# Performance work log

Hardware: AMD Instinct MI355X
Metric: run time of the kernel (lower is better)

The kernel has to match this reference:

```python
import jax, jax.numpy as jnp
import numpy as np

N, E, G, F, H, L, NH, HD = 40000, 640000, 256, 9, 128, 3, 4, 32
EPS = 1e-5

def _ln(x, g, b):
    m = jnp.mean(x, axis=-1, keepdims=True)
    v = jnp.mean((x - m) ** 2, axis=-1, keepdims=True)
    return (x - m) * jax.lax.rsqrt(v + EPS) * g + b

def _forward(floats, edge_index, batch):
    (x, pos, emb_w, emb_b, edge_w1, edge_b1, edge_w2, edge_b2,
     node_w1, node_b1, node_w2, node_b2, qkv_w, qkv_b, out_w, out_b,
     ln1_g, ln1_b, ln2_g, ln2_b, ff_w1, ff_b1, ff_w2, ff_b2,
     cls_w1, cls_b1, cls_w2, cls_b2) = floats
    src, dst = edge_index[0], edge_index[1]  # PyG: x_j = x[src], x_i = x[dst], aggregate at dst
    dist = jnp.linalg.norm(pos[dst] - pos[src], axis=-1, keepdims=True)  # [E,1]
    h = x @ emb_w + emb_b  # [N,H]
    for l in range(L):
        # message: edge_mlp(cat[x_i, x_j, dist])
        ef = jnp.concatenate([h[dst], h[src], dist], axis=-1)  # [E,2H+1]
        m = jax.nn.silu(ef @ edge_w1[l] + edge_b1[l])
        m = jax.nn.silu(m @ edge_w2[l] + edge_b2[l])  # [E,H]
        aggr = jax.ops.segment_sum(m, dst, num_segments=N)  # [N,H]
        u = jax.nn.silu(jnp.concatenate([h, aggr], axis=-1) @ node_w1[l] + node_b1[l])
        u = u @ node_w2[l] + node_b2[l]
        h = h + u  # residual in GAHT.forward
    # per-graph mean pooling (faithful to masked-mean loop)
    sums = jax.ops.segment_sum(h, batch, num_segments=G)  # [G,H]
    cnts = jax.ops.segment_sum(jnp.ones((N,), h.dtype), batch, num_segments=G)
    g = sums / jnp.maximum(cnts, 1.0)[:, None]  # [G,H]
    # 2-layer post-norm transformer encoder (batch=1, seq=G), relu FFN, eval mode (no dropout)
    scale = 1.0 / jnp.sqrt(jnp.asarray(HD, g.dtype))
    for t in range(2):
        qkv = g @ qkv_w[t] + qkv_b[t]  # [G,3H]
        q, k, v = jnp.split(qkv, 3, axis=-1)
        q = q.reshape(G, NH, HD); k = k.reshape(G, NH, HD); v = v.reshape(G, NH, HD)
        att = jax.nn.softmax(jnp.einsum('qhd,khd->hqk', q, k) * scale, axis=-1)
        o = jnp.einsum('hqk,khd->qhd', att, v).reshape(G, H)
        o = o @ out_w[t] + out_b[t]
        g = _ln(g + o, ln1_g[t], ln1_b[t])
        ff = jax.nn.relu(g @ ff_w1[t] + ff_b1[t]) @ ff_w2[t] + ff_b2[t]
        g = _ln(g + ff, ln2_g[t], ln2_b[t])
    out = jax.nn.relu(g @ cls_w1 + cls_b1) @ cls_w2 + cls_b2  # [G,1]
    return out.squeeze(-1)  # [G]


def setup_inputs() -> dict:
    key = jax.random.key(0)
    ks = jax.random.split(key, 16)
    def p(k, shape, scale=0.08):
        return jax.random.normal(k, shape, dtype=jnp.float32) * scale
    return {
        'x': jax.random.normal(ks[0], (N, F), dtype=jnp.float32),
        'pos': jax.random.normal(ks[1], (N, 3), dtype=jnp.float32),
        'emb_w': p(ks[2], (F, H)), 'emb_b': jnp.zeros((H,), jnp.float32),
        'edge_w1': p(ks[3], (L, 2 * H + 1, H)), 'edge_b1': jnp.zeros((L, H), jnp.float32),
        'edge_w2': p(ks[4], (L, H, H)), 'edge_b2': jnp.zeros((L, H), jnp.float32),
        'node_w1': p(ks[5], (L, 2 * H, H)), 'node_b1': jnp.zeros((L, H), jnp.float32),
        'node_w2': p(ks[6], (L, H, H)), 'node_b2': jnp.zeros((L, H), jnp.float32),
        'qkv_w': p(ks[7], (2, H, 3 * H)), 'qkv_b': jnp.zeros((2, 3 * H), jnp.float32),
        'out_w': p(ks[8], (2, H, H)), 'out_b': jnp.zeros((2, H), jnp.float32),
        'ln1_g': jnp.ones((2, H), jnp.float32), 'ln1_b': jnp.zeros((2, H), jnp.float32),
        'ln2_g': jnp.ones((2, H), jnp.float32), 'ln2_b': jnp.zeros((2, H), jnp.float32),
        'ff_w1': p(ks[9], (2, H, 2 * H)), 'ff_b1': jnp.zeros((2, 2 * H), jnp.float32),
        'ff_w2': p(ks[10], (2, 2 * H, H)), 'ff_b2': jnp.zeros((2, H), jnp.float32),
        'cls_w1': p(ks[11], (H, H // 2)), 'cls_b1': jnp.zeros((H // 2,), jnp.float32),
        'cls_w2': p(ks[12], (H // 2, 1)), 'cls_b2': jnp.zeros((1,), jnp.float32),
        'edge_index': jax.random.randint(ks[13], (2, E), 0, N),
        'batch': jnp.sort(jax.random.randint(ks[14], (N,), 0, G)),
    }


def reference(x, pos, emb_w, emb_b, edge_w1, edge_b1, edge_w2, edge_b2,
              node_w1, node_b1, node_w2, node_b2, qkv_w, qkv_b, out_w, out_b,
              ln1_g, ln1_b, ln2_g, ln2_b, ff_w1, ff_b1, ff_w2, ff_b2,
              cls_w1, cls_b1, cls_w2, cls_b2, edge_index, batch):
    floats = (x, pos, emb_w, emb_b, edge_w1, edge_b1, edge_w2, edge_b2,
              node_w1, node_b1, node_w2, node_b2, qkv_w, qkv_b, out_w, out_b,
              ln1_g, ln1_b, ln2_g, ln2_b, ff_w1, ff_b1, ff_w2, ff_b2,
              cls_w1, cls_b1, cls_w2, cls_b2)
    return _forward(floats, edge_index, batch)
```

## Files before the change

### kernel.cpp

```cpp
#include <hip/hip_runtime.h>
#include <hip/hip_bf16.h>
#include <stdint.h>

#define NN 40000
#define EE 640000
#define GG 256
#define FFE 9
#define HH 128

typedef __bf16 bf16;
typedef __bf16 bf16x8 __attribute__((ext_vector_type(8)));
typedef float f32x4 __attribute__((ext_vector_type(4)));

__device__ __forceinline__ f32x4 mfma16(bf16x8 a, bf16x8 b, f32x4 c){
  return __builtin_amdgcn_mfma_f32_16x16x32_bf16(a, b, c, 0, 0, 0);
}
__device__ __forceinline__ float silu_f(float x){
  return x * __builtin_amdgcn_rcpf(1.0f + __expf(-x));
}
__device__ __forceinline__ uint16_t bfb(float x){ bf16 h=(bf16)x; return *(uint16_t*)&h; }
__device__ __forceinline__ int swz(int row, int cb){
  return row*256 + (cb ^ ((row & 7) << 4));
}

__global__ __launch_bounds__(256) void k_prep(
    const float* __restrict__ edge_w1, const float* __restrict__ edge_w2,
    const float* __restrict__ node_w1, const float* __restrict__ node_w2,
    const float* __restrict__ edge_b1,
    const float* __restrict__ x, const float* __restrict__ emb_w,
    const float* __restrict__ emb_b,
    bf16* __restrict__ wcatT, bf16* __restrict__ w2T,
    bf16* __restrict__ nw1T, bf16* __restrict__ nw2T,
    float* __restrict__ bcat, float* __restrict__ h,
    int* __restrict__ cnt)
{
  int b = blockIdx.x, tid = threadIdx.x;
  if (b < 192){
    int l = b/64; int t2 = (b%64)*256 + tid;
    int n = t2 >> 7, k = t2 & 127;
    wcatT[(size_t)l*32768 + n*128 + k] = (bf16)edge_w1[(size_t)l*32896 + k*128 + n];
  } else if (b < 384){
    int lb = b - 192; int l = lb/64; int t2 = (lb%64)*256 + tid;
    int n = t2 >> 7, k = t2 & 127;
    wcatT[(size_t)l*32768 + 16384 + n*128 + k] = (bf16)edge_w1[(size_t)l*32896 + (128+k)*128 + n];
  } else if (b < 576){
    int lb = b - 384; int l = lb/64; int t2 = (lb%64)*256 + tid;
    int n = t2 >> 7, k = t2 & 127;
    w2T[(size_t)l*16384 + n*128 + k] = (bf16)edge_w2[(size_t)l*16384 + k*128 + n];
  } else if (b < 960){
    int lb = b - 576; int l = lb/128; int t2 = (lb%128)*256 + tid;
    int n = t2 >> 8, k = t2 & 255;
    nw1T[(size_t)l*32768 + n*256 + k] = (bf16)node_w1[(size_t)l*32768 + k*128 + n];
  } else if (b < 1152){
    int lb = b - 960; int l = lb/64; int t2 = (lb%64)*256 + tid;
    int n = t2 >> 7, k = t2 & 127;
    nw2T[(size_t)l*16384 + n*128 + k] = (bf16)node_w2[(size_t)l*16384 + k*128 + n];
  } else if (b < 1155){
    int l = b - 1152;
    bcat[l*256 + tid] = (tid < 128) ? edge_b1[l*128 + tid] : 0.0f;
  } else if (b < 1312){
    int i = (b - 1155)*256 + tid;
    if (i < NN) cnt[i] = 0;
  } else {
    int idx = (b - 1312)*256 + tid;
    int n = idx >> 7, f = idx & 127;
    float s = emb_b[f];
    const float* xr = x + n*FFE;
    #pragma unroll
    for (int k=0;k<FFE;++k) s += xr[k]*emb_w[k*HH + f];
    h[idx] = s;
  }
}

__global__ __launch_bounds__(256) void k_hist(const int* __restrict__ dst, int* __restrict__ cnt){
  int e = blockIdx.x*256 + threadIdx.x;
  if (e < EE) atomicAdd(&cnt[dst[e]], 1);
}

__global__ __launch_bounds__(1024) void k_scan(const int* __restrict__ cnt, int* __restrict__ cursor, int n){
  __shared__ int s_wsum[16];
  __shared__ int s_run;
  int tid = threadIdx.x, lane = tid & 63, wv = tid >> 6;
  if (tid == 0) s_run = 0;
  __syncthreads();
  for (int base=0; base<n; base+=4096){
    int i = base + tid*4;
    int c0 = (i  <n)? cnt[i  ] : 0;
    int c1 = (i+1<n)? cnt[i+1] : 0;
    int c2 = (i+2<n)? cnt[i+2] : 0;
    int c3 = (i+3<n)? cnt[i+3] : 0;
    int t0 = c0, t1 = t0+c1, t2 = t1+c2, t3 = t2+c3;
    int xx = t3;
    #pragma unroll
    for (int off=1; off<64; off<<=1){ int t = __shfl_up(xx, off); if (lane>=off) xx += t; }
    if (lane==63) s_wsum[wv] = xx;
    __syncthreads();
    if (wv==0 && lane<16){
      int y = s_wsum[lane];
      #pragma unroll
      for (int off=1; off<16; off<<=1){ int t = __shfl_up(y, off, 16); if (lane>=off) y += t; }
      s_wsum[lane] = y;
    }
    __syncthreads();
    int woff = wv ? s_wsum[wv-1] : 0;
    int run = s_run;
    int eb = run + woff + xx - t3;
    if (i  <n) cursor[i  ] = eb;
    if (i+1<n) cursor[i+1] = eb + t0;
    if (i+2<n) cursor[i+2] = eb + t1;
    if (i+3<n) cursor[i+3] = eb + t2;
    __syncthreads();
    if (tid==0) s_run = run + s_wsum[15];
    __syncthreads();
  }
}

__global__ __launch_bounds__(256) void k_scatter(
    const int* __restrict__ ei, const float* __restrict__ pos,
    int* __restrict__ cursor, int4* __restrict__ rec)
{
  int e = blockIdx.x*256 + threadIdx.x;
  if (e >= EE) return;
  int s = ei[e], d = ei[EE + e];
  int p = atomicAdd(&cursor[d], 1);
  float dx = pos[d*3+0]-pos[s*3+0];
  float dy = pos[d*3+1]-pos[s*3+1];
  float dz = pos[d*3+2]-pos[s*3+2];
  int4 rc; rc.x = s; rc.y = d; rc.z = __float_as_int(sqrtf(dx*dx+dy*dy+dz*dz)); rc.w = 0;
  rec[p] = rc;
}

template<int KTOT, int K1, int ACT, bool A1BF, bool BIAS, bool RESID, bool OBF, bool OF, bool ZAGGR>
__global__ __launch_bounds__(256) void k_gemm(
    const void* __restrict__ a1v, const float* __restrict__ a2,
    const bf16* __restrict__ wt, const float* __restrict__ bias,
    const float* __restrict__ resid, bf16* __restrict__ outb,
    float* __restrict__ outf, int Nw, float* __restrict__ aggr)
{
  constexpr int LDK = 136;
  __shared__ bf16 s_a[128*LDK];
  __shared__ bf16 s_w[64*LDK];
  int tid = threadIdx.x, lane = tid & 63, w = tid >> 6;
  int m0 = blockIdx.x*128, n0 = blockIdx.y*64;
  if (ZAGGR && blockIdx.y == 0){
    int nrows = NN - m0; if (nrows > 128) nrows = 128;
    f32x4 z = {0.f,0.f,0.f,0.f};
    for (int i = tid; i < nrows*32; i += 256)
      *(f32x4*)(aggr + (size_t)m0*128 + (size_t)i*4) = z;
  }
  f32x4 acc[2][4];
  #pragma unroll
  for (int i=0;i<2;++i)
    #pragma unroll
    for (int j=0;j<4;++j)
      #pragma unroll
      for (int r=0;r<4;++r) acc[i][j][r]=0.f;
  int rsel = lane & 15, ksel = (lane>>4)*8;
  int wm = w*32;

  for (int kh=0; kh<KTOT; kh+=128){
    #pragma unroll
    for (int it=0; it<8; ++it){
      int idx = tid + it*256;
      int row = idx >> 4, col = (idx & 15)*8;
      int gc = kh + col;
      int grow = m0 + row; if (grow > NN-1) grow = NN-1;
      bf16x8 vv;
      if (gc < K1){
        if (A1BF){
          vv = *(const bf16x8*)((const bf16*)a1v + (size_t)grow*K1 + gc);
        } else {
          const float* srcp = (const float*)a1v + (size_t)grow*K1 + gc;
          f32x4 u0 = *(const f32x4*)srcp;
          f32x4 u1 = *(const f32x4*)(srcp+4);
          vv[0]=(bf16)u0[0]; vv[1]=(bf16)u0[1]; vv[2]=(bf16)u0[2]; vv[3]=(bf16)u0[3];
          vv[4]=(bf16)u1[0]; vv[5]=(bf16)u1[1]; vv[6]=(bf16)u1[2]; vv[7]=(bf16)u1[3];
        }
      } else {
        const float* srcp = a2 + (size_t)grow*(KTOT-K1) + (gc-K1);
        f32x4 u0 = *(const f32x4*)srcp;
        f32x4 u1 = *(const f32x4*)(srcp+4);
        vv[0]=(bf16)u0[0]; vv[1]=(bf16)u0[1]; vv[2]=(bf16)u0[2]; vv[3]=(bf16)u0[3];
        vv[4]=(bf16)u1[0]; vv[5]=(bf16)u1[1]; vv[6]=(bf16)u1[2]; vv[7]=(bf16)u1[3];
      }
      *(bf16x8*)&s_a[row*LDK + col] = vv;
    }
    #pragma unroll
    for (int it=0; it<4; ++it){
      int idx = tid + it*256;
      int row = idx >> 4, col = (idx & 15)*8;
      *(bf16x8*)&s_w[row*LDK + col] = *(const bf16x8*)(wt + (size_t)(n0+row)*KTOT + kh + col);
    }
    __syncthreads();
    #pragma unroll
    for (int ks=0; ks<4; ++ks){
      int kb = ks*32 + ksel;
      bf16x8 fa0 = *(const bf16x8*)&s_a[(wm+rsel)*LDK + kb];
      bf16x8 fa1 = *(const bf16x8*)&s_a[(wm+16+rsel)*LDK + kb];
      #pragma unroll
      for (int j=0;j<4;++j){
        bf16x8 fb = *(const bf16x8*)&s_w[(j*16+rsel)*LDK + kb];
        acc[0][j]=mfma16(fa0,fb,acc[0][j]);
        acc[1][j]=mfma16(fa1,fb,acc[1][j]);
      }
    }
    __syncthreads();
  }

  #pragma unroll
  for (int i=0;i<2;++i){
    #pragma unroll
    for (int j=0;j<4;++j){
      int col = n0 + j*16 + rsel;
      float bv = BIAS ? bias[col] : 0.0f;
      #pragma unroll
      for (int r=0;r<4;++r){
        int row = m0 + wm + i*16 + 4*(lane>>4) + r;
        if (row < NN){
          float v = acc[i][j][r] + bv;
          if (ACT==1) v = silu_f(v);
          if (RESID) v += resid[(size_t)row*Nw + col];
          if (OBF) outb[(size_t)row*Nw + col] = (bf16)v;
          if (OF)  outf[(size_t)row*Nw + col] = v;
        }
      }
    }
  }
}

template<bool DOP>
__global__ __launch_bounds__(256) void k_node(
    float* h, float* aggr,
    const bf16* __restrict__ nw1t,
    const bf16* __restrict__ nw2t,
    const bf16* __restrict__ wct,
    const float* __restrict__ nb1, const float* __restrict__ nb2,
    const float* __restrict__ bcv,
    bf16* __restrict__ P)
{
  __shared__ bf16 SA[64][132];
  __shared__ bf16 SW[128][72];
  __shared__ bf16 SU[64][132];
  int tid = threadIdx.x, lane = tid & 63, w = tid >> 6;
  int rsel = lane & 15, hi = lane >> 4;
  int m0 = blockIdx.x * 64;
  int urow = w*16 + rsel;
  int grow = m0 + urow;

  f32x4 acc[8];
  #pragma unroll
  for (int nt=0;nt<8;++nt)
    #pragma unroll
    for (int r=0;r<4;++r) acc[nt][r]=0.f;

  for (int kq=0; kq<4; ++kq){
    const float* src = (kq < 2) ? (h + (size_t)m0*128 + kq*64)
                                : (aggr + (size_t)m0*128 + (kq-2)*64);
    #pragma unroll
    for (int it=0; it<2; ++it){
      int g = tid + it*256;
      int row = g >> 3, cg = (g & 7)*8;
      const float* sp = src + (size_t)row*128 + cg;
      f32x4 u0 = *(const f32x4*)sp, u1v = *(const f32x4*)(sp+4);
      bf16x8 vv;
      vv[0]=(bf16)u0[0]; vv[1]=(bf16)u0[1]; vv[2]=(bf16)u0[2]; vv[3]=(bf16)u0[3];
      vv[4]=(bf16)u1v[0]; vv[5]=(bf16)u1v[1]; vv[6]=(bf16)u1v[2]; vv[7]=(bf16)u1v[3];
      *(bf16x8*)&SA[row][cg] = vv;
    }
    #pragma unroll
    for (int it=0; it<4; ++it){
      int g = tid + it*256;
      int row = g >> 3, cg = (g & 7)*8;
      *(bf16x8*)&SW[row][cg] = *(const bf16x8*)(nw1t + (size_t)row*256 + kq*64 + cg);
    }
    __syncthreads();
    #pragma unroll
    for (int ks=0; ks<2; ++ks){
      int kb = ks*32 + hi*8;
      bf16x8 fa = *(const bf16x8*)&SA[w*16 + rsel][kb];
      #pragma unroll
      for (int nt=0;nt<8;++nt){
        bf16x8 fw = *(const bf16x8*)&SW[nt*16 + rsel][kb];
        acc[nt] = mfma16(fw, fa, acc[nt]);
      }
    }
    __syncthreads();
  }

  #pragma unroll
  for (int nt=0;nt<8;++nt){
    int nb = nt*16 + 4*hi;
    f32x4 b4 = *(const f32x4*)(nb1 + nb);
    uint16_t q0 = bfb(silu_f(acc[nt][0] + b4[0]));
    uint16_t q1 = bfb(silu_f(acc[nt][1] + b4[1]));
    uint16_t q2 = bfb(silu_f(acc[nt][2] + b4[2]));
    uint16_t q3 = bfb(silu_f(acc[nt][3] + b4[3]));
    uint2 pk; pk.x = (unsigned)q0 | ((unsigned)q1 << 16); pk.y = (unsigned)q2 | ((unsigned)q3 << 16);
    *(uint2*)&SU[urow][nb] = pk;
  }
  __syncthreads();

  #pragma unroll
  for (int nt=0;nt<8;++nt)
    #pragma unroll
    for (int r=0;r<4;++r) acc[nt][r]=0.f;
  for (int kq=0; kq<2; ++kq){
    #pragma unroll
    for (int it=0; it<4; ++it){
      int g = tid + it*256;
      int row = g >> 3, cg = (g & 7)*8;
      *(bf16x8*)&SW[row][cg] = *(const bf16x8*)(nw2t + (size_t)row*128 + kq*64 + cg);
    }
    __syncthreads();
    #pragma unroll
    for (int ks=0; ks<2; ++ks){
      int kb = ks*32 + hi*8;
      bf16x8 fa = *(const bf16x8*)&SU[w*16 + rsel][kq*64 + kb];
      #pragma unroll
      for (int nt=0;nt<8;++nt){
        bf16x8 fw = *(const bf16x8*)&SW[nt*16 + rsel][kb];
        acc[nt] = mfma16(fw, fa, acc[nt]);
      }
    }
    __syncthreads();
  }

  #pragma unroll
  for (int nt=0;nt<8;++nt){
    int nb = nt*16 + 4*hi;
    f32x4 b4 = *(const f32x4*)(nb2 + nb);
    f32x4 h4 = *(const f32x4*)(h + (size_t)grow*128 + nb);
    f32x4 v;
    #pragma unroll
    for (int r=0;r<4;++r) v[r] = h4[r] + acc[nt][r] + b4[r];
    *(f32x4*)(h + (size_t)grow*128 + nb) = v;
    uint2 pk;
    pk.x = (unsigned)bfb(v[0]) | ((unsigned)bfb(v[1]) << 16);
    pk.y = (unsigned)bfb(v[2]) | ((unsigned)bfb(v[3]) << 16);
    *(uint2*)&SA[urow][nb] = pk;
  }
  __syncthreads();

  if (DOP){
    for (int nh=0; nh<2; ++nh){
      #pragma unroll
      for (int nt=0;nt<8;++nt)
        #pragma unroll
        for (int r=0;r<4;++r) acc[nt][r]=0.f;
      for (int kq=0; kq<2; ++kq){
        #pragma unroll
        for (int it=0; it<4; ++it){
          int g = tid + it*256;
          int row = g >> 3, cg = (g & 7)*8;
          *(bf16x8*)&SW[row][cg] = *(const bf16x8*)(wct + (size_t)(nh*128+row)*128 + kq*64 + cg);
        }
        __syncthreads();
        #pragma unroll
        for (int ks=0; ks<2; ++ks){
          int kb = ks*32 + hi*8;
          bf16x8 fa = *(const bf16x8*)&SA[w*16 + rsel][kq*64 + kb];
          #pragma unroll
          for (int nt=0;nt<8;++nt){
            bf16x8 fw = *(const bf16x8*)&SW[nt*16 + rsel][kb];
            acc[nt] = mfma16(fw, fa, acc[nt]);
          }
        }
        __syncthreads();
      }
      #pragma unroll
      for (int nt=0;nt<8;++nt){
        int nb = nh*128 + nt*16 + 4*hi;
        f32x4 b4 = *(const f32x4*)(bcv + nb);
        uint2 pk;
        pk.x = (unsigned)bfb(acc[nt][0] + b4[0]) | ((unsigned)bfb(acc[nt][1] + b4[1]) << 16);
        pk.y = (unsigned)bfb(acc[nt][2] + b4[2]) | ((unsigned)bfb(acc[nt][3] + b4[3]) << 16);
        *(uint2*)(P + (size_t)grow*256 + nb) = pk;
      }
    }
    f32x4 z = {0.f,0.f,0.f,0.f};
    #pragma unroll
    for (int it=0; it<8; ++it){
      int idx = tid + it*256;
      *(f32x4*)(aggr + (size_t)m0*128 + (size_t)idx*4) = z;
    }
  }
}

__global__ __launch_bounds__(512, 6) void k_edge(
    const bf16* __restrict__ P, const bf16* __restrict__ w2t,
    const float* __restrict__ w1r, const float* __restrict__ b2,
    const int4* __restrict__ rec, float* __restrict__ aggr)
{
  __shared__ char smem[32768];
  __shared__ int s_dst[128];
  __shared__ unsigned s_segidw[32];
  __shared__ int s_segdst[128];
  __shared__ int s_misc[4];
  int tid = threadIdx.x, lane = tid & 63, w = tid >> 6;
  int rsel = lane & 15, hi = lane >> 4;
  int bid = blockIdx.x;
  int swb = (bid & 7) * (EE/128/8) + (bid >> 3);
  int e0 = swb * 128;
  int col = w*16 + rsel;

  bf16x8 fb[4];
  #pragma unroll
  for (int ks=0;ks<4;++ks)
    fb[ks] = *(const bf16x8*)(w2t + (size_t)col*128 + ks*32 + hi*8);

  if (tid == 0){
    s_misc[0] = (e0 == 0) ? -2147483647 : rec[e0-1].y;
    s_misc[1] = (e0 + 128 >= EE) ? -2147483647 : rec[e0+128].y;
  }

  int cq = (tid & 15)*8;
  int er = tid >> 4;
  int4 rc[4];
  #pragma unroll
  for (int it=0; it<4; ++it) rc[it] = rec[e0 + er + it*32];
  uint4 pau[4], pbu[4];
  #pragma unroll
  for (int it=0; it<4; ++it){
    pau[it] = *(const uint4*)(P + ((size_t)rc[it].y << 8) + cq);
    pbu[it] = *(const uint4*)(P + ((size_t)rc[it].x << 8) + 128 + cq);
  }
  if (cq == 0){
    #pragma unroll
    for (int it=0; it<4; ++it) s_dst[er + it*32] = rc[it].y;
  }
  f32x4 wr0 = *(const f32x4*)(w1r + cq);
  f32x4 wr1 = *(const f32x4*)(w1r + cq + 4);
  #pragma unroll
  for (int it=0; it<4; ++it){
    float dist = __int_as_float(rc[it].z);
    bf16x8 mm;
    #pragma unroll
    for (int j=0;j<4;++j){
      unsigned ua = ((const unsigned*)&pau[it])[j];
      unsigned ub = ((const unsigned*)&pbu[it])[j];
      float al = __uint_as_float(ua << 16);
      float ah = __uint_as_float(ua & 0xFFFF0000u);
      float bl = __uint_as_float(ub << 16);
      float bh = __uint_as_float(ub & 0xFFFF0000u);
      float wlo = (j<2) ? wr0[2*j]   : wr1[2*(j-2)];
      float whi = (j<2) ? wr0[2*j+1] : wr1[2*(j-2)+1];
      mm[2*j]   = (bf16)silu_f(al + bl + dist*wlo);
      mm[2*j+1] = (bf16)silu_f(ah + bh + dist*whi);
    }
    *(bf16x8*)(smem + swz(er + it*32, cq*2)) = mm;
  }
  __syncthreads();

  if (w == 0){
    int d0 = s_dst[2*lane], d1 = s_dst[2*lane+1];
    int dm1 = (lane == 0) ? 0 : s_dst[2*lane-1];
    int h0 = (lane == 0) ? 1 : (d0 != dm1);
    int h1 = (d1 != d0);
    int p = h0 + h1, x = p;
    #pragma unroll
    for (int off=1; off<64; off<<=1){ int t = __shfl_up(x, off); if (lane>=off) x += t; }
    int excl = x - p;
    int id0 = excl + h0 - 1;
    int id1 = excl + p - 1;
    uint8_t* sb = (uint8_t*)s_segidw;
    sb[2*lane]   = (uint8_t)id0;
    sb[2*lane+1] = (uint8_t)id1;
    if (h0) s_segdst[id0] = d0;
    if (h1) s_segdst[id1] = d1;
    if (lane == 63) s_misc[2] = id1 + 1;
  }

  f32x4 acc[8];
  #pragma unroll
  for (int mt=0;mt<8;++mt)
    #pragma unroll
    for (int r=0;r<4;++r) acc[mt][r]=0.f;
  #pragma unroll
  for (int mt=0;mt<8;++mt){
    #pragma unroll
    for (int ks=0;ks<4;++ks){
      bf16x8 fa = *(const bf16x8*)(smem + swz(mt*16 + rsel, ks*64 + hi*16));
      acc[mt] = mfma16(fa, fb[ks], acc[mt]);
    }
  }
  __syncthreads();

  float bb = b2[col];
  #pragma unroll
  for (int mt=0;mt<8;++mt){
    uint2 pk;
    pk.x = (unsigned)bfb(silu_f(acc[mt][0] + bb)) | ((unsigned)bfb(silu_f(acc[mt][1] + bb)) << 16);
    pk.y = (unsigned)bfb(silu_f(acc[mt][2] + bb)) | ((unsigned)bfb(silu_f(acc[mt][3] + bb)) << 16);
    *(uint2*)(smem + col*256 + ((mt*32 + hi*8) ^ ((col & 7) << 4))) = pk;
  }
  __syncthreads();

  bf16x8 gb[4];
  #pragma unroll
  for (int ks=0;ks<4;++ks)
    gb[ks] = *(const bf16x8*)(smem + col*256 + ((ks*64 + hi*16) ^ ((col & 7) << 4)));
  int nseg = s_misc[2];
  bool openL = (s_dst[0]   == s_misc[0]);
  bool openR = (s_dst[127] == s_misc[1]);
  for (int st = 0; st < nseg; st += 16){
    unsigned tgt = (unsigned)(st + rsel);
    f32x4 racc = {0.f,0.f,0.f,0.f};
    #pragma unroll
    for (int ks=0;ks<4;++ks){
      unsigned w0 = s_segidw[ks*8 + hi*2];
      unsigned w1 = s_segidw[ks*8 + hi*2 + 1];
      union { uint16_t u[8]; bf16x8 v; } sa;
      #pragma unroll
      for (int j=0;j<4;++j){
        sa.u[j]   = (((w0 >> (8*j)) & 255u) == tgt) ? (uint16_t)0x3F80 : (uint16_t)0;
        sa.u[4+j] = (((w1 >> (8*j)) & 255u) == tgt) ? (uint16_t)0x3F80 : (uint16_t)0;
      }
      racc = mfma16(sa.v, gb[ks], racc);
    }
    #pragma unroll
    for (int r=0;r<4;++r){
      int s = st + 4*hi + r;
      if (s < nseg){
        float v = racc[r];
        size_t off = (size_t)s_segdst[s]*128 + col;
        bool atom = (s == 0 && openL) || (s == nseg-1 && openR);
        if (atom) atomicAdd(&aggr[off], v);
        else      aggr[off] = v;
      }
    }
  }
}

__device__ __forceinline__ int lbound(const int* a, int n, int key){
  int lo=0, hi=n;
  while (lo<hi){ int mid=(lo+hi)>>1; if (a[mid]<key) lo=mid+1; else hi=mid; }
  return lo;
}

__global__ __launch_bounds__(384) void k_pool_qkv(
    const float* __restrict__ h, const int* __restrict__ batch,
    const float* __restrict__ wq, const float* __restrict__ bq,
    float* __restrict__ gbuf, float* __restrict__ qkvb)
{
  __shared__ float sg[128];
  int gr = blockIdx.x, tid = threadIdx.x;
  if (tid < 128){
    int lo = lbound(batch, NN, gr), hi2 = lbound(batch, NN, gr+1);
    float s = 0.f;
    for (int n=lo;n<hi2;++n) s += h[(size_t)n*HH + tid];
    int c = hi2 - lo; if (c < 1) c = 1;
    s /= (float)c;
    sg[tid] = s; gbuf[gr*128 + tid] = s;
  }
  __syncthreads();
  float a = bq[tid];
  for (int k=0;k<128;++k) a += sg[k]*wq[k*384 + tid];
  qkvb[gr*384 + tid] = a;
}

template<int MODE>
__global__ __launch_bounds__(128) void k_tail(
    const float* __restrict__ qkv, const float* __restrict__ wo,
    const float* __restrict__ bo, const float* __restrict__ l1g,
    const float* __restrict__ l1b, const float* __restrict__ w1,
    const float* __restrict__ b1f, const float* __restrict__ w2,
    const float* __restrict__ b2f, const float* __restrict__ l2g,
    const float* __restrict__ l2b, float* __restrict__ gbuf,
    const float* __restrict__ wq2, const float* __restrict__ bq2,
    float* __restrict__ qkvb2,
    const float* __restrict__ cw1, const float* __restrict__ cb1,
    const float* __restrict__ cw2, const float* __restrict__ cb2,
    float* __restrict__ out)
{
  __shared__ float sq[128];
  __shared__ float ss[4][256];
  __shared__ float so[128];
  __shared__ float st[256];
  __shared__ float red[4];
  int r = blockIdx.x, tid = threadIdx.x;
  sq[tid] = qkv[r*384 + tid];
  __syncthreads();
  const float scale = 0.17677669529663687f;
  for (int i=tid; i<1024; i+=128){
    int hh = i >> 8, j = i & 255;
    const float* kr = qkv + j*384 + 128 + hh*32;
    const float* qr = sq + hh*32;
    float s=0;
    #pragma unroll
    for (int d=0;d<32;++d) s += qr[d]*kr[d];
    ss[hh][j] = s*scale;
  }
  __syncthreads();
  int hh = tid >> 5, sl = tid & 31;
  float m = -1e30f;
  #pragma unroll
  for (int q8=0;q8<8;++q8) m = fmaxf(m, ss[hh][sl + q8*32]);
  #pragma unroll
  for (int off=16; off; off>>=1) m = fmaxf(m, __shfl_xor(m, off, 32));
  float sum = 0.f;
  #pragma unroll
  for (int q8=0;q8<8;++q8){
    float e = __expf(ss[hh][sl+q8*32] - m);
    ss[hh][sl+q8*32] = e;
    sum += e;
  }
  #pragma unroll
  for (int off=16; off; off>>=1) sum += __shfl_xor(sum, off, 32);
  float inv = __builtin_amdgcn_rcpf(sum);
  __syncthreads();
  float accv = 0.f;
  for (int j=0;j<256;++j) accv += ss[hh][j]*qkv[j*384 + 256 + hh*32 + sl];
  so[tid] = accv*inv;
  __syncthreads();
  float a = bo[tid];
  for (int k=0;k<128;++k) a += so[k]*wo[k*128 + tid];
  float val = gbuf[r*128 + tid] + a;
  {
    float s = val, q = val*val;
    #pragma unroll
    for (int off=32; off; off>>=1){ s += __shfl_xor(s, off); q += __shfl_xor(q, off); }
    int lane = tid & 63, wv = tid >> 6;
    if (lane==0){ red[wv*2]=s; red[wv*2+1]=q; }
    __syncthreads();
    float S = red[0]+red[2], Q = red[1]+red[3];
    float mean = S*(1.0f/128.0f);
    float var = Q*(1.0f/128.0f) - mean*mean;
    float ninv = rsqrtf(var + 1e-5f);
    val = (val-mean)*ninv*l1g[tid] + l1b[tid];
  }
  sq[tid] = val;
  __syncthreads();
  float a0 = b1f[tid], a1 = b1f[tid+128];
  for (int k=0;k<128;++k){
    float gv = sq[k];
    a0 += gv*w1[k*256 + tid];
    a1 += gv*w1[k*256 + tid + 128];
  }
  st[tid]     = fmaxf(a0, 0.f);
  st[tid+128] = fmaxf(a1, 0.f);
  __syncthreads();
  float b = b2f[tid];
  for (int k=0;k<256;++k) b += st[k]*w2[k*128 + tid];
  float val2 = val + b;
  {
    float s = val2, q = val2*val2;
    #pragma unroll
    for (int off=32; off; off>>=1){ s += __shfl_xor(s, off); q += __shfl_xor(q, off); }
    int lane = tid & 63, wv = tid >> 6;
    __syncthreads();
    if (lane==0){ red[wv*2]=s; red[wv*2+1]=q; }
    __syncthreads();
    float S = red[0]+red[2], Q = red[1]+red[3];
    float mean = S*(1.0f/128.0f);
    float var = Q*(1.0f/128.0f) - mean*mean;
    float ninv = rsqrtf(var + 1e-5f);
    val2 = (val2-mean)*ninv*l2g[tid] + l2b[tid];
  }
  gbuf[r*128 + tid] = val2;
  if (MODE == 0){
    sq[tid] = val2;
    __syncthreads();
    float q0 = bq2[tid], q1 = bq2[tid+128], q2 = bq2[tid+256];
    for (int k=0;k<128;++k){
      float gv = sq[k];
      const float* wr = wq2 + k*384;
      q0 += gv*wr[tid]; q1 += gv*wr[tid+128]; q2 += gv*wr[tid+256];
    }
    qkvb2[r*384+tid]=q0; qkvb2[r*384+tid+128]=q1; qkvb2[r*384+tid+256]=q2;
  }
  if (MODE == 1){
    so[tid] = val2;
    __syncthreads();
    if (tid < 64){
      float c = cb1[tid];
      for (int k=0;k<128;++k) c += so[k]*cw1[k*64 + tid];
      c = fmaxf(c, 0.f);
      float p = c * cw2[tid];
      #pragma unroll
      for (int off=32; off; off>>=1) p += __shfl_xor(p, off);
      if (tid==0) out[r] = p + cb2[0];
    }
  }
}

extern "C" void kernel_launch(void* const* d_in, const int* in_sizes, int n_in,
                              void* d_out, int out_size, void* d_ws, size_t ws_size,
                              hipStream_t stream)
{
  (void)in_sizes; (void)n_in; (void)out_size; (void)ws_size;
  const float* x      = (const float*)d_in[0];
  const float* pos    = (const float*)d_in[1];
  const float* emb_w  = (const float*)d_in[2];
  const float* emb_b  = (const float*)d_in[3];
  const float* edge_w1= (const float*)d_in[4];
  const float* edge_b1= (const float*)d_in[5];
  const float* edge_w2= (const float*)d_in[6];
  const float* edge_b2= (const float*)d_in[7];
  const float* node_w1= (const float*)d_in[8];
  const float* node_b1= (const float*)d_in[9];
  const float* node_w2= (const float*)d_in[10];
  const float* node_b2= (const float*)d_in[11];
  const float* qkv_w  = (const float*)d_in[12];
  const float* qkv_b  = (const float*)d_in[13];
  const float* out_w  = (const float*)d_in[14];
  const float* out_b  = (const float*)d_in[15];
  const float* ln1_g  = (const float*)d_in[16];
  const float* ln1_b  = (const float*)d_in[17];
  const float* ln2_g  = (const float*)d_in[18];
  const float* ln2_b  = (const float*)d_in[19];
  const float* ff_w1  = (const float*)d_in[20];
  const float* ff_b1  = (const float*)d_in[21];
  const float* ff_w2  = (const float*)d_in[22];
  const float* ff_b2  = (const float*)d_in[23];
  const float* cls_w1 = (const float*)d_in[24];
  const float* cls_b1 = (const float*)d_in[25];
  const float* cls_w2 = (const float*)d_in[26];
  const float* cls_b2 = (const float*)d_in[27];
  const int* ei       = (const int*)d_in[28];
  const int* batch    = (const int*)d_in[29];
  float* out = (float*)d_out;

  uint8_t* wp = (uint8_t*)d_ws;
  auto take = [&](size_t nb)->void*{ void* r = wp; wp += (nb + 255) & ~(size_t)255; return r; };
  float* h      = (float*)take((size_t)NN*HH*4);
  bf16*  P      = (bf16*) take((size_t)NN*256*2);
  float* aggr   = (float*)take((size_t)NN*HH*4);
  int*   cnt    = (int*)  take((size_t)NN*4);
  int*   cursor = (int*)  take((size_t)NN*4);
  int4*  rec    = (int4*) take((size_t)EE*16);
  bf16*  wcatT  = (bf16*) take((size_t)3*256*128*2);
  bf16*  w2T    = (bf16*) take((size_t)3*128*128*2);
  bf16*  nw1T   = (bf16*) take((size_t)3*128*256*2);
  bf16*  nw2T   = (bf16*) take((size_t)3*128*128*2);
  float* bcat   = (float*)take((size_t)3*256*4);
  float* gbuf   = (float*)take((size_t)GG*HH*4);
  float* qkvb   = (float*)take((size_t)GG*384*4);
  float* qkvb2  = (float*)take((size_t)GG*384*4);

  dim3 b256(256);
  k_prep<<<dim3(21312), b256, 0, stream>>>(edge_w1, edge_w2, node_w1, node_w2,
    edge_b1, x, emb_w, emb_b, wcatT, w2T, nw1T, nw2T, bcat, h, cnt);
  k_hist<<<dim3(EE/256), b256, 0, stream>>>(ei + EE, cnt);
  k_scan<<<dim3(1), dim3(1024), 0, stream>>>(cnt, cursor, NN);
  k_scatter<<<dim3(EE/256), b256, 0, stream>>>(ei, pos, cursor, rec);

  k_gemm<128,128,0,false,true,false,true,false,true><<<dim3(313,4), b256, 0, stream>>>(
    h, nullptr, wcatT, bcat, nullptr, P, nullptr, 256, aggr);

  for (int l=0;l<3;++l){
    k_edge<<<dim3(EE/128), dim3(512), 0, stream>>>(P, w2T + (size_t)l*16384,
      edge_w1 + ((size_t)l*257 + 256)*128, edge_b2 + (size_t)l*128, rec, aggr);
    if (l < 2){
      k_node<true><<<dim3(625), b256, 0, stream>>>(h, aggr,
        nw1T + (size_t)l*32768, nw2T + (size_t)l*16384, wcatT + (size_t)(l+1)*32768,
        node_b1 + (size_t)l*128, node_b2 + (size_t)l*128, bcat + (size_t)(l+1)*256, P);
    } else {
      k_node<false><<<dim3(625), b256, 0, stream>>>(h, aggr,
        nw1T + (size_t)l*32768, nw2T + (size_t)l*16384, wcatT,
        node_b1 + (size_t)l*128, node_b2 + (size_t)l*128, bcat, P);
    }
  }

  k_pool_qkv<<<dim3(GG), dim3(384), 0, stream>>>(h, batch, qkv_w, qkv_b, gbuf, qkvb);
  k_tail<0><<<dim3(GG), dim3(128), 0, stream>>>(qkvb, out_w, out_b,
    ln1_g, ln1_b, ff_w1, ff_b1, ff_w2, ff_b2, ln2_g, ln2_b, gbuf,
    qkv_w + (size_t)128*384, qkv_b + 384, qkvb2,
    nullptr, nullptr, nullptr, nullptr, nullptr);
  k_tail<1><<<dim3(GG), dim3(128), 0, stream>>>(qkvb2, out_w + (size_t)128*128, out_b + 128,
    ln1_g + 128, ln1_b + 128, ff_w1 + (size_t)128*256, ff_b1 + 256,
    ff_w2 + (size_t)256*128, ff_b2 + 128, ln2_g + 128, ln2_b + 128, gbuf,
    nullptr, nullptr, nullptr,
    cls_w1, cls_b1, cls_w2, cls_b2, out);
}
```

Baseline: 669.1 us.

## Parallelize prefix scan, specialize initial P GEMM, precompute segment selector in LDS

Replaces the single-block sequential prefix scan with a two-pass multi-block scan (per-block partials plus a small second pass whose offsets are added in scatter). Replaces the generic templated GEMM for the initial projection with a dedicated 64-row kernel that computes all 256 outputs per block. In the edge kernel, builds the one-hot segment selector matrix in shared memory once per 16-segment tile rather than unpacking bytes per lane. This trades one extra tiny launch and extra barriers in the edge loop for less serialization in the scan and simpler GEMM code.

```diff
diff --git a/kernel.cpp b/kernel.cpp
--- a/kernel.cpp
+++ b/kernel.cpp
@@ -77,52 +77,55 @@
   if (e < EE) atomicAdd(&cnt[dst[e]], 1);
 }
 
-__global__ __launch_bounds__(1024) void k_scan(const int* __restrict__ cnt, int* __restrict__ cursor, int n){
+__global__ __launch_bounds__(1024) void k_scanA(const int* __restrict__ cnt,
+    int* __restrict__ cursor, int* __restrict__ partials, int n)
+{
   __shared__ int s_wsum[16];
-  __shared__ int s_run;
   int tid = threadIdx.x, lane = tid & 63, wv = tid >> 6;
-  if (tid == 0) s_run = 0;
-  __syncthreads();
-  for (int base=0; base<n; base+=4096){
-    int i = base + tid*4;
-    int c0 = (i  <n)? cnt[i  ] : 0;
-    int c1 = (i+1<n)? cnt[i+1] : 0;
-    int c2 = (i+2<n)? cnt[i+2] : 0;
-    int c3 = (i+3<n)? cnt[i+3] : 0;
-    int t0 = c0, t1 = t0+c1, t2 = t1+c2, t3 = t2+c3;
-    int xx = t3;
-    #pragma unroll
-    for (int off=1; off<64; off<<=1){ int t = __shfl_up(xx, off); if (lane>=off) xx += t; }
-    if (lane==63) s_wsum[wv] = xx;
-    __syncthreads();
-    if (wv==0 && lane<16){
-      int y = s_wsum[lane];
-      #pragma unroll
-      for (int off=1; off<16; off<<=1){ int t = __shfl_up(y, off, 16); if (lane>=off) y += t; }
-      s_wsum[lane] = y;
-    }
-    __syncthreads();
-    int woff = wv ? s_wsum[wv-1] : 0;
-    int run = s_run;
-    int eb = run + woff + xx - t3;
-    if (i  <n) cursor[i  ] = eb;
-    if (i+1<n) cursor[i+1] = eb + t0;
-    if (i+2<n) cursor[i+2] = eb + t1;
-    if (i+3<n) cursor[i+3] = eb + t2;
-    __syncthreads();
-    if (tid==0) s_run = run + s_wsum[15];
-    __syncthreads();
-  }
+  int i = blockIdx.x*4096 + tid*4;
+  int c0 = (i  <n)? cnt[i  ] : 0;
+  int c1 = (i+1<n)? cnt[i+1] : 0;
+  int c2 = (i+2<n)? cnt[i+2] : 0;
+  int c3 = (i+3<n)? cnt[i+3] : 0;
+  int t0 = c0, t1 = t0+c1, t2 = t1+c2, t3 = t2+c3;
+  int xx = t3;
+  #pragma unroll
+  for (int off=1; off<64; off<<=1){ int t = __shfl_up(xx, off); if (lane>=off) xx += t; }
+  if (lane==63) s_wsum[wv] = xx;
+  __syncthreads();
+  if (wv==0 && lane<16){
+    int y = s_wsum[lane];
+    #pragma unroll
+    for (int off=1; off<16; off<<=1){ int t = __shfl_up(y, off, 16); if (lane>=off) y += t; }
+    s_wsum[lane] = y;
+  }
+  __syncthreads();
+  int woff = wv ? s_wsum[wv-1] : 0;
+  int eb = woff + xx - t3;
+  if (i  <n) cursor[i  ] = eb;
+  if (i+1<n) cursor[i+1] = eb + t0;
+  if (i+2<n) cursor[i+2] = eb + t1;
+  if (i+3<n) cursor[i+3] = eb + t2;
+  if (tid==1023) partials[blockIdx.x] = woff + xx;
+}
+
+__global__ __launch_bounds__(64) void k_scanB(int* __restrict__ partials, int nb){
+  int lane = threadIdx.x;
+  int v = (lane < nb) ? partials[lane] : 0;
+  int x = v;
+  #pragma unroll
+  for (int off=1; off<64; off<<=1){ int t = __shfl_up(x, off); if (lane>=off) x += t; }
+  if (lane < nb) partials[lane] = x - v;
 }
 
 __global__ __launch_bounds__(256) void k_scatter(
     const int* __restrict__ ei, const float* __restrict__ pos,
-    int* __restrict__ cursor, int4* __restrict__ rec)
+    int* __restrict__ cursor, const int* __restrict__ offs, int4* __restrict__ rec)
 {
   int e = blockIdx.x*256 + threadIdx.x;
   if (e >= EE) return;
   int s = ei[e], d = ei[EE + e];
-  int p = atomicAdd(&cursor[d], 1);
+  int p = atomicAdd(&cursor[d], 1) + offs[d >> 12];
   float dx = pos[d*3+0]-pos[s*3+0];
   float dy = pos[d*3+1]-pos[s*3+1];
   float dz = pos[d*3+2]-pos[s*3+2];
@@ -130,100 +133,64 @@
   rec[p] = rc;
 }
 
-template<int KTOT, int K1, int ACT, bool A1BF, bool BIAS, bool RESID, bool OBF, bool OF, bool ZAGGR>
-__global__ __launch_bounds__(256) void k_gemm(
-    const void* __restrict__ a1v, const float* __restrict__ a2,
-    const bf16* __restrict__ wt, const float* __restrict__ bias,
-    const float* __restrict__ resid, bf16* __restrict__ outb,
-    float* __restrict__ outf, int Nw, float* __restrict__ aggr)
-{
-  constexpr int LDK = 136;
-  __shared__ bf16 s_a[128*LDK];
-  __shared__ bf16 s_w[64*LDK];
+__global__ __launch_bounds__(256) void k_pgen(
+    const float* __restrict__ h, const bf16* __restrict__ wct,
+    const float* __restrict__ bcv, bf16* __restrict__ P, float* __restrict__ aggr)
+{
+  __shared__ bf16 SA[64][136];
+  __shared__ bf16 SW[128][136];
   int tid = threadIdx.x, lane = tid & 63, w = tid >> 6;
-  int m0 = blockIdx.x*128, n0 = blockIdx.y*64;
-  if (ZAGGR && blockIdx.y == 0){
-    int nrows = NN - m0; if (nrows > 128) nrows = 128;
-    f32x4 z = {0.f,0.f,0.f,0.f};
-    for (int i = tid; i < nrows*32; i += 256)
-      *(f32x4*)(aggr + (size_t)m0*128 + (size_t)i*4) = z;
-  }
-  f32x4 acc[2][4];
-  #pragma unroll
-  for (int i=0;i<2;++i)
-    #pragma unroll
-    for (int j=0;j<4;++j)
-      #pragma unroll
-      for (int r=0;r<4;++r) acc[i][j][r]=0.f;
-  int rsel = lane & 15, ksel = (lane>>4)*8;
-  int wm = w*32;
-
-  for (int kh=0; kh<KTOT; kh+=128){
+  int rsel = lane & 15, hi = lane >> 4;
+  int m0 = blockIdx.x * 64;
+  f32x4 z = {0.f,0.f,0.f,0.f};
+  #pragma unroll
+  for (int it=0; it<8; ++it)
+    *(f32x4*)(aggr + (size_t)m0*128 + (size_t)(tid + it*256)*4) = z;
+  #pragma unroll
+  for (int it=0; it<4; ++it){
+    int idx = tid + it*256;
+    int row = idx >> 4, cg = (idx & 15)*8;
+    const float* sp = h + (size_t)(m0+row)*128 + cg;
+    f32x4 u0 = *(const f32x4*)sp, u1v = *(const f32x4*)(sp+4);
+    bf16x8 vv;
+    vv[0]=(bf16)u0[0]; vv[1]=(bf16)u0[1]; vv[2]=(bf16)u0[2]; vv[3]=(bf16)u0[3];
+    vv[4]=(bf16)u1v[0]; vv[5]=(bf16)u1v[1]; vv[6]=(bf16)u1v[2]; vv[7]=(bf16)u1v[3];
+    *(bf16x8*)&SA[row][cg] = vv;
+  }
+  __syncthreads();
+  int urow = w*16 + rsel;
+  for (int nh=0; nh<2; ++nh){
     #pragma unroll
     for (int it=0; it<8; ++it){
       int idx = tid + it*256;
-      int row = idx >> 4, col = (idx & 15)*8;
-      int gc = kh + col;
-      int grow = m0 + row; if (grow > NN-1) grow = NN-1;
-      bf16x8 vv;
-      if (gc < K1){
-        if (A1BF){
-          vv = *(const bf16x8*)((const bf16*)a1v + (size_t)grow*K1 + gc);
-        } else {
-          const float* srcp = (const float*)a1v + (size_t)grow*K1 + gc;
-          f32x4 u0 = *(const f32x4*)srcp;
-          f32x4 u1 = *(const f32x4*)(srcp+4);
-          vv[0]=(bf16)u0[0]; vv[1]=(bf16)u0[1]; vv[2]=(bf16)u0[2]; vv[3]=(bf16)u0[3];
-          vv[4]=(bf16)u1[0]; vv[5]=(bf16)u1[1]; vv[6]=(bf16)u1[2]; vv[7]=(bf16)u1[3];
-        }
-      } else {
-        const float* srcp = a2 + (size_t)grow*(KTOT-K1) + (gc-K1);
-        f32x4 u0 = *(const f32x4*)srcp;
-        f32x4 u1 = *(const f32x4*)(srcp+4);
-        vv[0]=(bf16)u0[0]; vv[1]=(bf16)u0[1]; vv[2]=(bf16)u0[2]; vv[3]=(bf16)u0[3];
-        vv[4]=(bf16)u1[0]; vv[5]=(bf16)u1[1]; vv[6]=(bf16)u1[2]; vv[7]=(bf16)u1[3];
+      int row = idx >> 4, cg = (idx & 15)*8;
+      *(bf16x8*)&SW[row][cg] = *(const bf16x8*)(wct + (size_t)(nh*128+row)*128 + cg);
+    }
+    __syncthreads();
+    f32x4 acc[8];
+    #pragma unroll
+    for (int nt=0;nt<8;++nt)
+      #pragma unroll
+      for (int r=0;r<4;++r) acc[nt][r]=0.f;
+    #pragma unroll
+    for (int ks=0; ks<4; ++ks){
+      int kb = ks*32 + hi*8;
+      bf16x8 fa = *(const bf16x8*)&SA[urow][kb];
+      #pragma unroll
+      for (int nt=0;nt<8;++nt){
+        bf16x8 fw = *(const bf16x8*)&SW[nt*16 + rsel][kb];
+        acc[nt] = mfma16(fw, fa, acc[nt]);
       }
-      *(bf16x8*)&s_a[row*LDK + col] = vv;
-    }
-    #pragma unroll
-    for (int it=0; it<4; ++it){
-      int idx = tid + it*256;
-      int row = idx >> 4, col = (idx & 15)*8;
-      *(bf16x8*)&s_w[row*LDK + col] = *(const bf16x8*)(wt + (size_t)(n0+row)*KTOT + kh + col);
-    }
-    __syncthreads();
-    #pragma unroll
-    for (int ks=0; ks<4; ++ks){
-      int kb = ks*32 + ksel;
-      bf16x8 fa0 = *(const bf16x8*)&s_a[(wm+rsel)*LDK + kb];
-      bf16x8 fa1 = *(const bf16x8*)&s_a[(wm+16+rsel)*LDK + kb];
-      #pragma unroll
-      for (int j=0;j<4;++j){
-        bf16x8 fb = *(const bf16x8*)&s_w[(j*16+rsel)*LDK + kb];
-        acc[0][j]=mfma16(fa0,fb,acc[0][j]);
-        acc[1][j]=mfma16(fa1,fb,acc[1][j]);
-      }
-    }
-    __syncthreads();
-  }
-
-  #pragma unroll
-  for (int i=0;i<2;++i){
-    #pragma unroll
-    for (int j=0;j<4;++j){
-      int col = n0 + j*16 + rsel;
-      float bv = BIAS ? bias[col] : 0.0f;
-      #pragma unroll
-      for (int r=0;r<4;++r){
-        int row = m0 + wm + i*16 + 4*(lane>>4) + r;
-        if (row < NN){
-          float v = acc[i][j][r] + bv;
-          if (ACT==1) v = silu_f(v);
-          if (RESID) v += resid[(size_t)row*Nw + col];
-          if (OBF) outb[(size_t)row*Nw + col] = (bf16)v;
-          if (OF)  outf[(size_t)row*Nw + col] = v;
-        }
-      }
+    }
+    __syncthreads();
+    #pragma unroll
+    for (int nt=0;nt<8;++nt){
+      int nb = nh*128 + nt*16 + 4*hi;
+      f32x4 b4 = *(const f32x4*)(bcv + nb);
+      uint2 pk;
+      pk.x = (unsigned)bfb(acc[nt][0] + b4[0]) | ((unsigned)bfb(acc[nt][1] + b4[1]) << 16);
+      pk.y = (unsigned)bfb(acc[nt][2] + b4[2]) | ((unsigned)bfb(acc[nt][3] + b4[3]) << 16);
+      *(uint2*)(P + (size_t)(m0+urow)*256 + nb) = pk;
     }
   }
 }
@@ -291,11 +258,9 @@
   for (int nt=0;nt<8;++nt){
     int nb = nt*16 + 4*hi;
     f32x4 b4 = *(const f32x4*)(nb1 + nb);
-    uint16_t q0 = bfb(silu_f(acc[nt][0] + b4[0]));
-    uint16_t q1 = bfb(silu_f(acc[nt][1] + b4[1]));
-    uint16_t q2 = bfb(silu_f(acc[nt][2] + b4[2]));
-    uint16_t q3 = bfb(silu_f(acc[nt][3] + b4[3]));
-    uint2 pk; pk.x = (unsigned)q0 | ((unsigned)q1 << 16); pk.y = (unsigned)q2 | ((unsigned)q3 << 16);
+    uint2 pk;
+    pk.x = (unsigned)bfb(silu_f(acc[nt][0] + b4[0])) | ((unsigned)bfb(silu_f(acc[nt][1] + b4[1])) << 16);
+    pk.y = (unsigned)bfb(silu_f(acc[nt][2] + b4[2])) | ((unsigned)bfb(silu_f(acc[nt][3] + b4[3])) << 16);
     *(uint2*)&SU[urow][nb] = pk;
   }
   __syncthreads();
@@ -393,8 +358,9 @@
 {
   __shared__ char smem[32768];
   __shared__ int s_dst[128];
-  __shared__ unsigned s_segidw[32];
+  __shared__ int s_segid[128];
   __shared__ int s_segdst[128];
+  __shared__ bf16 s_sel[16][136];
   __shared__ int s_misc[4];
   int tid = threadIdx.x, lane = tid & 63, w = tid >> 6;
   int rsel = lane & 15, hi = lane >> 4;
@@ -462,9 +428,8 @@
     int excl = x - p;
     int id0 = excl + h0 - 1;
     int id1 = excl + p - 1;
-    uint8_t* sb = (uint8_t*)s_segidw;
-    sb[2*lane]   = (uint8_t)id0;
-    sb[2*lane+1] = (uint8_t)id1;
+    s_segid[2*lane]   = id0;
+    s_segid[2*lane+1] = id1;
     if (h0) s_segdst[id0] = d0;
     if (h1) s_segdst[id1] = d1;
     if (lane == 63) s_misc[2] = id1 + 1;
@@ -502,20 +467,21 @@
   int nseg = s_misc[2];
   bool openL = (s_dst[0]   == s_misc[0]);
   bool openR = (s_dst[127] == s_misc[1]);
+  const bf16 ONE = (bf16)1.0f, ZERO = (bf16)0.0f;
   for (int st = 0; st < nseg; st += 16){
-    unsigned tgt = (unsigned)(st + rsel);
+    __syncthreads();
+    #pragma unroll
+    for (int k4=0;k4<4;++k4){
+      int idx = tid + k4*512;
+      int s = idx >> 7, e = idx & 127;
+      s_sel[s][e] = (s_segid[e] == st + s) ? ONE : ZERO;
+    }
+    __syncthreads();
     f32x4 racc = {0.f,0.f,0.f,0.f};
     #pragma unroll
     for (int ks=0;ks<4;++ks){
-      unsigned w0 = s_segidw[ks*8 + hi*2];
-      unsigned w1 = s_segidw[ks*8 + hi*2 + 1];
-      union { uint16_t u[8]; bf16x8 v; } sa;
-      #pragma unroll
-      for (int j=0;j<4;++j){
-        sa.u[j]   = (((w0 >> (8*j)) & 255u) == tgt) ? (uint16_t)0x3F80 : (uint16_t)0;
-        sa.u[4+j] = (((w1 >> (8*j)) & 255u) == tgt) ? (uint16_t)0x3F80 : (uint16_t)0;
-      }
-      racc = mfma16(sa.v, gb[ks], racc);
+      bf16x8 sa = *(const bf16x8*)&s_sel[rsel][ks*32 + hi*8];
+      racc = mfma16(sa, gb[ks], racc);
     }
     #pragma unroll
     for (int r=0;r<4;++r){
@@ -727,6 +693,7 @@
   float* aggr   = (float*)take((size_t)NN*HH*4);
   int*   cnt    = (int*)  take((size_t)NN*4);
   int*   cursor = (int*)  take((size_t)NN*4);
+  int*   parts  = (int*)  take((size_t)64*4);
   int4*  rec    = (int4*) take((size_t)EE*16);
   bf16*  wcatT  = (bf16*) take((size_t)3*256*128*2);
   bf16*  w2T    = (bf16*) take((size_t)3*128*128*2);
@@ -741,11 +708,11 @@
   k_prep<<<dim3(21312), b256, 0, stream>>>(edge_w1, edge_w2, node_w1, node_w2,
     edge_b1, x, emb_w, emb_b, wcatT, w2T, nw1T, nw2T, bcat, h, cnt);
   k_hist<<<dim3(EE/256), b256, 0, stream>>>(ei + EE, cnt);
-  k_scan<<<dim3(1), dim3(1024), 0, stream>>>(cnt, cursor, NN);
-  k_scatter<<<dim3(EE/256), b256, 0, stream>>>(ei, pos, cursor, rec);
-
-  k_gemm<128,128,0,false,true,false,true,false,true><<<dim3(313,4), b256, 0, stream>>>(
-    h, nullptr, wcatT, bcat, nullptr, P, nullptr, 256, aggr);
+  k_scanA<<<dim3(10), dim3(1024), 0, stream>>>(cnt, cursor, parts, NN);
+  k_scanB<<<dim3(1), dim3(64), 0, stream>>>(parts, 10);
+  k_scatter<<<dim3(EE/256), b256, 0, stream>>>(ei, pos, cursor, parts, rec);
+
+  k_pgen<<<dim3(625), b256, 0, stream>>>(h, wcatT, bcat, P, aggr);
 
   for (int l=0;l<3;++l){
     k_edge<<<dim3(EE/128), dim3(512), 0, stream>>>(P, w2T + (size_t)l*16384,
```

New measurement: 631.3 us. -5.6%, faster.
